# Kernel tuning notes

Hardware: AMD Instinct MI355X
Metric: run time of the kernel (lower is better)

The kernel has to match this reference:

```python
import jax, jax.numpy as jnp
import numpy as np


def _nn_sq_dists(query, ref):
    # query: [B, N, 3], ref: [B, M, 3]
    # squared distance via ||q||^2 + ||r||^2 - 2 q.r, min over ref points
    q2 = jnp.sum(query * query, axis=-1)            # [B, N]
    r2 = jnp.sum(ref * ref, axis=-1)                # [B, M]
    cross = jnp.einsum('bnc,bmc->bnm', query, ref)  # [B, N, M]
    d = q2[:, :, None] + r2[:, None, :] - 2.0 * cross
    d = jnp.maximum(d, 0.0)  # clamp numerical negatives (true distances >= 0)
    return jnp.min(d, axis=-1)                      # [B, N] 1-NN squared dists


def setup_inputs() -> dict:
    key = jax.random.key(0)
    k1, k2 = jax.random.split(key)
    B, C, N = 4, 3, 8192
    pc2 = jax.random.normal(k1, (B, C, N), dtype=jnp.float32)
    pc1_warped = jax.random.normal(k2, (B, C, N), dtype=jnp.float32)
    return {"pc2": pc2, "pc1_warped": pc1_warped}


def reference(pc2, pc1_warped):
    # pos1 = target['pc2'], pos2 = output['pc1_warped'], both [B, 3, N]
    pos1 = jnp.transpose(pc2, (0, 2, 1))         # [B, N, 3]
    pos2 = jnp.transpose(pc1_warped, (0, 2, 1))  # [B, N, 3]
    # pointutils.knn(1, pos1, pos2): for each pos1 point, nearest in pos2.
    nn_d = _nn_sq_dists(pos1, pos2)              # [B, N]
    per_batch = jnp.sum(nn_d, axis=1)            # sum over dim 1
    loss = per_batch.mean() + per_batch.mean()
    return loss
```

## Files before the change

kernel.cpp:

```cpp
#include <hip/hip_runtime.h>


#define NPTS  8192
#define NB    4
#define NCH   256
#define RR    8
#define RCPR  32
#define QPB   4

typedef float f32x16 __attribute__((ext_vector_type(16)));
typedef short bf16x8 __attribute__((ext_vector_type(8)));

static __device__ __forceinline__ unsigned int f2bf(float f) {
    unsigned int u = __float_as_uint(f);
    u += 0x7FFF + ((u >> 16) & 1);
    return u >> 16;
}
static __device__ __forceinline__ float bf2f(unsigned int s) {
    return __uint_as_float(s << 16);
}

__global__ __launch_bounds__(256) void chamfer_prep(
    const float* __restrict__ pc2,
    const float* __restrict__ pc1w,
    uint4* __restrict__ qfrag, uint4* __restrict__ rfrag,
    float* __restrict__ out)
{
    int t = blockIdx.x * 256 + threadIdx.x;
    if (t == 0) out[0] = 0.0f;
    int side = t >> 15;
    int rem  = t & 32767;
    int b = rem >> 13;
    int n = rem & 8191;
    const float* src = (side ? pc1w : pc2) + b * 3 * NPTS;
    float x = src[n], y = src[NPTS + n], z = src[2 * NPTS + n];
    unsigned int xh = f2bf(x), yh = f2bf(y), zh = f2bf(z);
    unsigned int xl = f2bf(x - bf2f(xh));
    unsigned int yl = f2bf(y - bf2f(yh));
    unsigned int zl = f2bf(z - bf2f(zh));
    int chunk = n >> 5, lane = n & 31;
    uint4 g0, g1;
    if (side == 0) {
        g0.x = xh | (xh << 16);
        g0.y = xl | (yh << 16);
        g0.z = yh | (yl << 16);
        g0.w = zh | (zh << 16);
        g1.x = zl | (0x3F80u << 16);
        g1.y = 0x3F80u;
        g1.z = 0u; g1.w = 0u;
    } else {
        float h = -0.5f * (x * x + y * y + z * z);
        unsigned int hh = f2bf(h);
        unsigned int hl = f2bf(h - bf2f(hh));
        g0.x = xh | (xl << 16);
        g0.y = xh | (yh << 16);
        g0.z = yl | (yh << 16);
        g0.w = zh | (zl << 16);
        g1.x = zh | (hh << 16);
        g1.y = hl;
        g1.z = 0u; g1.w = 0u;
    }
    uint4* dst = (side ? rfrag : qfrag) + ((b * NCH + chunk) * 64 + lane);
    dst[0]  = g0;
    dst[32] = g1;
}

__global__ __launch_bounds__(256) void chamfer_mfma(
    const uint4* __restrict__ qfrag, const uint4* __restrict__ rfrag,
    float* __restrict__ partial)
{
    __shared__ uint4 slds[2048];
    const int tid  = threadIdx.x;
    const int b    = blockIdx.z;
    const int rr   = blockIdx.y;
    const int wave = tid >> 6;
    const int lane = tid & 63;

    const uint4* rsrc = rfrag + (b * NCH + rr * RCPR) * 64;
#pragma unroll
    for (int i = 0; i < 8; ++i)
        slds[tid + i * 256] = rsrc[tid + i * 256];
    __syncthreads();

    const int qc = blockIdx.x * QPB + wave;
    uint4 bq_u = qfrag[(b * NCH + qc) * 64 + (lane >> 5) * 32 + (lane & 31)];
    bf16x8 bq = __builtin_bit_cast(bf16x8, bq_u);

    f32x16 zero;
#pragma unroll
    for (int i = 0; i < 16; ++i) zero[i] = 0.0f;

    float rm0 = -3e38f, rm1 = -3e38f, rm2 = -3e38f, rm3 = -3e38f;
    const int abase = (lane >> 5) * 32 + (lane & 31);
#pragma unroll 2
    for (int c = 0; c < RCPR; ++c) {
        bf16x8 a = __builtin_bit_cast(bf16x8, slds[c * 64 + abase]);
        f32x16 d = __builtin_amdgcn_mfma_f32_32x32x16_bf16(a, bq, zero, 0, 0, 0);
        rm0 = fmaxf(rm0, fmaxf(d[0],  d[1]));
        rm0 = fmaxf(rm0, fmaxf(d[2],  d[3]));
        rm1 = fmaxf(rm1, fmaxf(d[4],  d[5]));
        rm1 = fmaxf(rm1, fmaxf(d[6],  d[7]));
        rm2 = fmaxf(rm2, fmaxf(d[8],  d[9]));
        rm2 = fmaxf(rm2, fmaxf(d[10], d[11]));
        rm3 = fmaxf(rm3, fmaxf(d[12], d[13]));
        rm3 = fmaxf(rm3, fmaxf(d[14], d[15]));
    }
    float rm = fmaxf(fmaxf(rm0, rm1), fmaxf(rm2, rm3));
    rm = fmaxf(rm, __shfl_xor(rm, 32, 64));
    if (lane < 32)
        partial[(b * RR + rr) * NPTS + qc * 32 + lane] = rm;
}

__global__ __launch_bounds__(512) void chamfer_reduce(
    const float* __restrict__ pc2,
    const float* __restrict__ partial,
    float* __restrict__ out)
{
    const int g = blockIdx.x * 512 + threadIdx.x;
    const int b = g >> 13, n = g & 8191;
    float smax = -3e38f;
#pragma unroll
    for (int c = 0; c < RR; ++c)
        smax = fmaxf(smax, partial[(b * RR + c) * NPTS + n]);

    const float* qb = pc2 + b * 3 * NPTS;
    float qx = qb[n], qy = qb[NPTS + n], qz = qb[2 * NPTS + n];
    float q2 = qx * qx + qy * qy + qz * qz;
    float d = fmaxf(q2 - 2.0f * smax, 0.0f);

#pragma unroll
    for (int off = 32; off > 0; off >>= 1)
        d += __shfl_down(d, off, 64);

    __shared__ float wsum[8];
    const int lane = threadIdx.x & 63;
    const int wid  = threadIdx.x >> 6;
    if (lane == 0) wsum[wid] = d;
    __syncthreads();
    if (threadIdx.x == 0) {
        float s = 0.0f;
#pragma unroll
        for (int w = 0; w < 8; ++w) s += wsum[w];
        atomicAdd(out, s * (2.0f / NB));
    }
}

extern "C" void kernel_launch(void* const* d_in, const int* in_sizes, int n_in,
                              void* d_out, int out_size, void* d_ws, size_t ws_size,
                              hipStream_t stream) {
    const float* pc2  = (const float*)d_in[0];
    const float* pc1w = (const float*)d_in[1];
    float* out = (float*)d_out;
    uint4* qfrag   = (uint4*)d_ws;
    uint4* rfrag   = (uint4*)((char*)d_ws + (1u << 20));
    float* partial = (float*)((char*)d_ws + (2u << 20));

    chamfer_prep<<<256, 256, 0, stream>>>(pc2, pc1w, qfrag, rfrag, out);
    dim3 g1(NCH / QPB, RR, NB);
    chamfer_mfma<<<g1, 256, 0, stream>>>(qfrag, rfrag, partial);
    chamfer_reduce<<<NB * NPTS / 512, 512, 0, stream>>>(pc2, partial, out);
}
```

Before: 78.99 us.

## Fuse bf16 fragment prep into MFMA kernel and use 8-wave blocks

Drops the separate prep kernel. Each MFMA block now converts its reference slice from raw fp32 into split-bf16 fragments straight into LDS, and each wave builds its query fragment in registers. Blocks grow from 4 to 8 waves so every LDS reference tile serves more query chunks. This removes one launch and the workspace round trip. The cost is that reference conversion is repeated in every block that shares the same reference slice, and the grid holds fewer, larger blocks.

```diff
diff --git a/kernel.cpp b/kernel.cpp
--- a/kernel.cpp
+++ b/kernel.cpp
@@ -6,7 +6,8 @@
 #define NCH   256
 #define RR    8
 #define RCPR  32
-#define QPB   4
+#define WPB   8
+#define BT    (WPB*64)
 
 typedef float f32x16 __attribute__((ext_vector_type(16)));
 typedef short bf16x8 __attribute__((ext_vector_type(8)));
@@ -20,71 +21,58 @@
     return __uint_as_float(s << 16);
 }
 
-__global__ __launch_bounds__(256) void chamfer_prep(
+__global__ __launch_bounds__(BT) void chamfer_mfma(
     const float* __restrict__ pc2,
     const float* __restrict__ pc1w,
-    uint4* __restrict__ qfrag, uint4* __restrict__ rfrag,
+    float* __restrict__ partial,
     float* __restrict__ out)
 {
-    int t = blockIdx.x * 256 + threadIdx.x;
-    if (t == 0) out[0] = 0.0f;
-    int side = t >> 15;
-    int rem  = t & 32767;
-    int b = rem >> 13;
-    int n = rem & 8191;
-    const float* src = (side ? pc1w : pc2) + b * 3 * NPTS;
-    float x = src[n], y = src[NPTS + n], z = src[2 * NPTS + n];
-    unsigned int xh = f2bf(x), yh = f2bf(y), zh = f2bf(z);
-    unsigned int xl = f2bf(x - bf2f(xh));
-    unsigned int yl = f2bf(y - bf2f(yh));
-    unsigned int zl = f2bf(z - bf2f(zh));
-    int chunk = n >> 5, lane = n & 31;
-    uint4 g0, g1;
-    if (side == 0) {
-        g0.x = xh | (xh << 16);
-        g0.y = xl | (yh << 16);
-        g0.z = yh | (yl << 16);
-        g0.w = zh | (zh << 16);
-        g1.x = zl | (0x3F80u << 16);
-        g1.y = 0x3F80u;
-        g1.z = 0u; g1.w = 0u;
-    } else {
-        float h = -0.5f * (x * x + y * y + z * z);
-        unsigned int hh = f2bf(h);
-        unsigned int hl = f2bf(h - bf2f(hh));
-        g0.x = xh | (xl << 16);
-        g0.y = xh | (yh << 16);
-        g0.z = yl | (yh << 16);
-        g0.w = zh | (zl << 16);
-        g1.x = zh | (hh << 16);
-        g1.y = hl;
-        g1.z = 0u; g1.w = 0u;
-    }
-    uint4* dst = (side ? rfrag : qfrag) + ((b * NCH + chunk) * 64 + lane);
-    dst[0]  = g0;
-    dst[32] = g1;
-}
-
-__global__ __launch_bounds__(256) void chamfer_mfma(
-    const uint4* __restrict__ qfrag, const uint4* __restrict__ rfrag,
-    float* __restrict__ partial)
-{
-    __shared__ uint4 slds[2048];
+    __shared__ uint4 slds[RCPR * 64];
     const int tid  = threadIdx.x;
     const int b    = blockIdx.z;
     const int rr   = blockIdx.y;
     const int wave = tid >> 6;
     const int lane = tid & 63;
 
-    const uint4* rsrc = rfrag + (b * NCH + rr * RCPR) * 64;
+    if (blockIdx.x == 0 && rr == 0 && b == 0 && tid == 0)
+        out[0] = 0.0f;
+
+    const float* refb = pc1w + b * 3 * NPTS + rr * (RCPR * 32);
 #pragma unroll
-    for (int i = 0; i < 8; ++i)
-        slds[tid + i * 256] = rsrc[tid + i * 256];
+    for (int j = 0; j < 2; ++j) {
+        int i = tid + j * BT;
+        float x = refb[i], y = refb[NPTS + i], z = refb[2 * NPTS + i];
+        unsigned xh = f2bf(x), yh = f2bf(y), zh = f2bf(z);
+        unsigned xl = f2bf(x - bf2f(xh));
+        unsigned yl = f2bf(y - bf2f(yh));
+        unsigned zl = f2bf(z - bf2f(zh));
+        float h = -0.5f * (x * x + y * y + z * z);
+        unsigned hh = f2bf(h);
+        unsigned hl = f2bf(h - bf2f(hh));
+        int c = i >> 5, l32 = i & 31;
+        slds[c * 64 + l32] =
+            make_uint4(xh | (xl << 16), xh | (yh << 16),
+                       yl | (yh << 16), zh | (zl << 16));
+        slds[c * 64 + 32 + l32] = make_uint4(zh | (hh << 16), hl, 0u, 0u);
+    }
+
+    const int qc = blockIdx.x * WPB + wave;
+    const int qn = qc * 32 + (lane & 31);
+    const float* qb = pc2 + b * 3 * NPTS;
+    {
+    }
+    float x = qb[qn], y = qb[NPTS + qn], z = qb[2 * NPTS + qn];
+    unsigned xh = f2bf(x), yh = f2bf(y), zh = f2bf(z);
+    unsigned xl = f2bf(x - bf2f(xh));
+    unsigned yl = f2bf(y - bf2f(yh));
+    unsigned zl = f2bf(z - bf2f(zh));
+    uint4 bu = (lane < 32)
+        ? make_uint4(xh | (xh << 16), xl | (yh << 16),
+                     yh | (yl << 16), zh | (zh << 16))
+        : make_uint4(zl | (0x3F80u << 16), 0x3F80u, 0u, 0u);
+    bf16x8 bq = __builtin_bit_cast(bf16x8, bu);
+
     __syncthreads();
-
-    const int qc = blockIdx.x * QPB + wave;
-    uint4 bq_u = qfrag[(b * NCH + qc) * 64 + (lane >> 5) * 32 + (lane & 31)];
-    bf16x8 bq = __builtin_bit_cast(bf16x8, bq_u);
 
     f32x16 zero;
 #pragma unroll
@@ -151,12 +139,9 @@
     const float* pc2  = (const float*)d_in[0];
     const float* pc1w = (const float*)d_in[1];
     float* out = (float*)d_out;
-    uint4* qfrag   = (uint4*)d_ws;
-    uint4* rfrag   = (uint4*)((char*)d_ws + (1u << 20));
-    float* partial = (float*)((char*)d_ws + (2u << 20));
+    float* partial = (float*)d_ws;
 
-    chamfer_prep<<<256, 256, 0, stream>>>(pc2, pc1w, qfrag, rfrag, out);
-    dim3 g1(NCH / QPB, RR, NB);
-    chamfer_mfma<<<g1, 256, 0, stream>>>(qfrag, rfrag, partial);
+    dim3 g1(NCH / WPB, RR, NB);
+    chamfer_mfma<<<g1, BT, 0, stream>>>(pc2, pc1w, partial, out);
     chamfer_reduce<<<NB * NPTS / 512, 512, 0, stream>>>(pc2, partial, out);
 }
```

After: 74.82 us. -5.3%, faster.
